# Performance work log

Measured on AMD Instinct MI355X. Metric: run time of the kernel, lower is better.

The kernel has to match this reference:

```python
import jax, jax.numpy as jnp
import numpy as np

EPS = 0.01       # l2-normalize epsilon
BN_EPS = 0.001   # batchnorm epsilon

def _l2norm(u):
    # tf.math.l2_normalize over axis=-2: x / sqrt(max(sum(x^2), eps))
    sq = jnp.sum(u * u, axis=-2, keepdims=True)
    return u / jnp.sqrt(jnp.maximum(sq, EPS))

def _dotprod(t, u):
    # einsum '...ij,...ik->...jk' contracting spatial axis, then flatten (C,C)->C*C
    d = jnp.einsum('bndi,bndj->bnij', t, _l2norm(u))
    return d.reshape(d.shape[0], d.shape[1], -1)

def _bn(x, gamma, beta):
    # inference-mode BN with moving_mean=0, moving_var=1 (fresh init)
    return gamma * (x / jnp.sqrt(1.0 + BN_EPS)) + beta

def setup_inputs() -> dict:
    key = jax.random.key(0)
    ks = jax.random.split(key, 9)
    B, N, D, C, BAS, U_IN, U_EQ = 8, 1024, 3, 64, 16, 512, 64
    F = 2 * C * C  # 8192 invariant features (2 input heads)
    t1 = jax.random.normal(ks[0], (B, N, D, C), dtype=jnp.float32)
    t2 = jax.random.normal(ks[1], (B, N, D, C), dtype=jnp.float32)
    u1 = jax.random.normal(ks[2], (B, N, D, C), dtype=jnp.float32)
    u2 = jax.random.normal(ks[3], (B, N, D, C), dtype=jnp.float32)
    V1 = jax.random.normal(ks[4], (B, N, D, BAS), dtype=jnp.float32)
    V2 = jax.random.normal(ks[5], (B, N, D, BAS), dtype=jnp.float32)
    W_inv = jax.random.normal(ks[6], (F, U_IN), dtype=jnp.float32) * 0.02
    b_inv = jnp.zeros((U_IN,), dtype=jnp.float32)
    g_inv = jnp.ones((U_IN,), dtype=jnp.float32)
    be_inv = jnp.zeros((U_IN,), dtype=jnp.float32)
    # two equivariant heads, each Dense(units=U_EQ*BAS)
    W_eq = jax.random.normal(ks[7], (2, F, U_EQ * BAS), dtype=jnp.float32) * 0.02
    b_eq = jnp.zeros((2, U_EQ * BAS), dtype=jnp.float32)
    g_eq = jnp.ones((2, U_EQ * BAS), dtype=jnp.float32)
    be_eq = jnp.zeros((2, U_EQ * BAS), dtype=jnp.float32)
    return {"t1": t1, "t2": t2, "u1": u1, "u2": u2, "V1": V1, "V2": V2,
            "W_inv": W_inv, "b_inv": b_inv, "g_inv": g_inv, "be_inv": be_inv,
            "W_eq": W_eq, "b_eq": b_eq, "g_eq": g_eq, "be_eq": be_eq}

def reference(t1, t2, u1, u2, V1, V2, W_inv, b_inv, g_inv, be_inv,
              W_eq, b_eq, g_eq, be_eq):
    # invariant features: concatenated flattened Gram blocks of the two heads
    feats = jnp.concatenate([_dotprod(t1, u1), _dotprod(t2, u2)], axis=-1)  # (B,N,F)
    # invariant branch: Dense -> BN -> ReLU
    invar = jax.nn.relu(_bn(feats @ W_inv + b_inv, g_inv, be_inv))  # (B,N,U_IN)
    # equivariant branch per head: Dense -> BN -> ReLU -> reshape -> basis recombine
    bas = V1.shape[-1]
    u_eq = W_eq.shape[-1] // bas
    eq_outs = []
    for l, V in enumerate((V1, V2)):
        wl = jax.nn.relu(_bn(feats @ W_eq[l] + b_eq[l], g_eq[l], be_eq[l]))
        wl = wl.reshape(wl.shape[0], wl.shape[1], u_eq, bas)  # (B,N,units,basis)
        # einsum '...ij,...mj->...mi': combine basis vectors -> (B,N,3,units)
        eq_outs.append(jnp.einsum('bnij,bnmj->bnmi', wl, V))
    eqvar = jnp.concatenate(eq_outs, axis=-1)  # (B,N,3,2*units)
    return invar, eqvar
```

## Files before the change

### kernel.cpp

```cpp
#include <hip/hip_runtime.h>
#include <hip/hip_bf16.h>

#define BROWS 8192
#define DDIM 3
#define CDIM 64
#define KF 8192
#define NINV 512
#define NEQ 1024
#define NTOT 2560
#define BAS 16
#define UEQ 64


typedef float f32x4 __attribute__((ext_vector_type(4)));
typedef __bf16 bf16x8_t __attribute__((ext_vector_type(8)));
typedef __bf16 bf16x4_t __attribute__((ext_vector_type(4)));

__device__ __forceinline__ void async_copy16(const void* g, void* l) {
    __builtin_amdgcn_global_load_lds(
        (__attribute__((address_space(1))) void*)(g),
        (__attribute__((address_space(3))) void*)(l), 16, 0, 0);
}

__global__ __launch_bounds__(256) void feats_kernel(
    const float* __restrict__ t1, const float* __restrict__ t2,
    const float* __restrict__ u1, const float* __restrict__ u2,
    __hip_bfloat16* __restrict__ feats)
{
    const int row = blockIdx.x;
    const int tid = threadIdx.x;
    __shared__ float sT[2 * DDIM * CDIM];
    __shared__ float sU[2 * DDIM * CDIM];

    const size_t base = (size_t)row * (DDIM * CDIM);
    if (tid < 192) {
        sT[tid]       = t1[base + tid];
        sT[192 + tid] = t2[base + tid];
        sU[tid]       = u1[base + tid];
        sU[192 + tid] = u2[base + tid];
    }
    __syncthreads();
    if (tid < 128) {
        const int h = tid >> 6, c = tid & 63;
        float* U = sU + h * 192;
        float sq = U[c] * U[c] + U[64 + c] * U[64 + c] + U[128 + c] * U[128 + c];
        float s = 1.0f / sqrtf(fmaxf(sq, 0.01f));
        U[c] *= s; U[64 + c] *= s; U[128 + c] *= s;
    }
    __syncthreads();
    const int h  = tid >> 7;
    const int i  = (tid >> 1) & 63;
    const int jh = (tid & 1) * 32;
    const float* T = sT + h * 192;
    const float* U = sU + h * 192;
    const float ti0 = T[i], ti1 = T[64 + i], ti2 = T[128 + i];

    const int kbase = h * 4096 + i * 64 + jh;
    const int kt    = kbase >> 5;
    const int mb    = row >> 8, rloc = row & 255;
    char* line = (char*)feats + (((size_t)(mb * 256 + kt)) << 14) + rloc * 64;

    #pragma unroll
    for (int g = 0; g < 4; ++g) {
        const int phys = (g + (rloc >> 1)) & 3;
        #pragma unroll
        for (int half = 0; half < 2; ++half) {
            const int j = jh + g * 8 + half * 4;
            const float4 u0 = *reinterpret_cast<const float4*>(U + j);
            const float4 u1 = *reinterpret_cast<const float4*>(U + 64 + j);
            const float4 u2 = *reinterpret_cast<const float4*>(U + 128 + j);
            bf16x4_t v;
            v[0] = (__bf16)(ti0 * u0.x + ti1 * u1.x + ti2 * u2.x);
            v[1] = (__bf16)(ti0 * u0.y + ti1 * u1.y + ti2 * u2.y);
            v[2] = (__bf16)(ti0 * u0.z + ti1 * u1.z + ti2 * u2.z);
            v[3] = (__bf16)(ti0 * u0.w + ti1 * u1.w + ti2 * u2.w);
            *reinterpret_cast<bf16x4_t*>(line + phys * 16 + half * 8) = v;
        }
    }
}

__global__ __launch_bounds__(256) void wt_kernel(
    const float* __restrict__ W_inv, const float* __restrict__ W_eq,
    __hip_bfloat16* __restrict__ WT)
{
    __shared__ float tile[32][33];
    const int tid = threadIdx.x;
    const int tx = tid & 31;
    const int ty = tid >> 5;
    const int n0 = blockIdx.x * 32;
    const int k0 = blockIdx.y * 32;

    const float* src; int ldn, nl0;
    if (n0 < NINV)            { src = W_inv;                       ldn = NINV; nl0 = n0; }
    else if (n0 < NINV + NEQ) { src = W_eq;                        ldn = NEQ;  nl0 = n0 - NINV; }
    else                      { src = W_eq + (size_t)KF * NEQ;     ldn = NEQ;  nl0 = n0 - NINV - NEQ; }

    #pragma unroll
    for (int i = 0; i < 4; ++i) {
        int kl = ty + i * 8;
        tile[kl][tx] = src[(size_t)(k0 + kl) * ldn + nl0 + tx];
    }
    __syncthreads();
    const int n_l = tid >> 3;
    const int k4  = (tid & 7) * 4;
    bf16x4_t v;
    #pragma unroll
    for (int q = 0; q < 4; ++q) v[q] = (__bf16)tile[k4 + q][n_l];

    const int n    = n0 + n_l;
    const int nb   = n >> 8, rloc = n & 255;
    const int kt   = k0 >> 5;
    const int lc   = (k4 >> 3) & 3, e = k4 & 7;
    const int phys = (lc + (rloc >> 1)) & 3;
    char* dst = (char*)WT + (((size_t)(nb * 256 + kt)) << 14)
              + rloc * 64 + phys * 16 + e * 2;
    *reinterpret_cast<bf16x4_t*>(dst) = v;
}

#define BM 256
#define BN 256
#define BK 32

struct GemmCtx {
    const char* pA;
    const char* pB;
    __hip_bfloat16* As[2];
    __hip_bfloat16* Bs[2];
    int soff;
    int chnk;
    int wm, wn, lane;
};

__device__ __forceinline__ void issue4(const GemmCtx& c, int buf, size_t toff) {
    #pragma unroll
    for (int j = 0; j < 2; ++j)
        async_copy16(c.pA + toff + c.soff + j * 8192,
                     (char*)c.As[buf] + c.soff + j * 8192);
    #pragma unroll
    for (int j = 0; j < 2; ++j)
        async_copy16(c.pB + toff + c.soff + j * 8192,
                     (char*)c.Bs[buf] + c.soff + j * 8192);
}

__device__ __forceinline__ void compute32(const GemmCtx& c, int buf, f32x4 (&acc)[4][8]) {
    const int l15 = c.lane & 15;
    bf16x8_t a[4], b[8];
    #pragma unroll
    for (int mt = 0; mt < 4; ++mt)
        a[mt] = *reinterpret_cast<const bf16x8_t*>(
            &c.As[buf][(c.wm + mt * 16 + l15) * BK + c.chnk]);
    #pragma unroll
    for (int nt = 0; nt < 8; ++nt)
        b[nt] = *reinterpret_cast<const bf16x8_t*>(
            &c.Bs[buf][(c.wn + nt * 16 + l15) * BK + c.chnk]);
    #pragma unroll
    for (int mt = 0; mt < 4; ++mt)
        #pragma unroll
        for (int nt = 0; nt < 8; ++nt)
            acc[mt][nt] = __builtin_amdgcn_mfma_f32_16x16x32_bf16(
                a[mt], b[nt], acc[mt][nt], 0, 0, 0);
}

__global__ __launch_bounds__(512, 2) void gemm_kernel(
    const __hip_bfloat16* __restrict__ A,
    const __hip_bfloat16* __restrict__ BT,
    const float* __restrict__ b_inv, const float* __restrict__ g_inv,
    const float* __restrict__ be_inv,
    const float* __restrict__ b_eq,  const float* __restrict__ g_eq,
    const float* __restrict__ be_eq,
    float* __restrict__ out_inv,
    float* __restrict__ Yeq)
{
    __shared__ alignas(16) __hip_bfloat16 AsBuf[2][BM * BK];
    __shared__ alignas(16) __hip_bfloat16 BsBuf[2][BN * BK];

    const int tid  = threadIdx.x;
    const int wave = tid >> 6;
    const int lane = tid & 63;

    const int b    = blockIdx.x;
    const int xcd  = b & 7;
    const int slot = b >> 3;
    const int nb   = slot % 10;
    const int mb   = xcd * 4 + slot / 10;
    const int n0   = nb * BN;
    const int m0   = mb * BM;

    GemmCtx c;
    c.wm   = (wave & 3) * 64;
    c.wn   = (wave >> 2) * 128;
    c.lane = lane;
    c.As[0] = &AsBuf[0][0]; c.As[1] = &AsBuf[1][0];
    c.Bs[0] = &BsBuf[0][0]; c.Bs[1] = &BsBuf[1][0];
    c.pA = (const char*)A  + ((size_t)mb << 22);
    c.pB = (const char*)BT + ((size_t)nb << 22);
    c.soff = tid * 16;
    c.chnk = (((lane >> 4) + ((lane & 15) >> 1)) & 3) * 8;

    f32x4 acc[4][8] = {};

    issue4(c, 0, 0);

    for (int kt = 0; kt < 256; kt += 2) {
        issue4(c, 1, ((size_t)(kt + 1)) << 14);
        asm volatile("s_waitcnt vmcnt(4)" ::: "memory");
        __builtin_amdgcn_s_barrier();
        asm volatile("" ::: "memory");
        compute32(c, 0, acc);
        asm volatile("" ::: "memory");
        __builtin_amdgcn_s_barrier();

        if (kt + 2 < 256) {
            issue4(c, 0, ((size_t)(kt + 2)) << 14);
            asm volatile("s_waitcnt vmcnt(4)" ::: "memory");
        } else {
            asm volatile("s_waitcnt vmcnt(0)" ::: "memory");
        }
        __builtin_amdgcn_s_barrier();
        asm volatile("" ::: "memory");
        compute32(c, 1, acc);
        asm volatile("" ::: "memory");
        __builtin_amdgcn_s_barrier();
    }

    const float RSQ = 0.9995003746877732f;
    #pragma unroll
    for (int nt = 0; nt < 8; ++nt) {
        const int gn = n0 + c.wn + nt * 16 + (lane & 15);
        float bbp, gg, bep;
        if (gn < NINV) {
            bbp = b_inv[gn]; gg = g_inv[gn]; bep = be_inv[gn];
        } else {
            const int e = gn - NINV, hh = e >> 10, nl = e & 1023;
            bbp = b_eq[hh * NEQ + nl]; gg = g_eq[hh * NEQ + nl]; bep = be_eq[hh * NEQ + nl];
        }
        gg *= RSQ;
        #pragma unroll
        for (int mt = 0; mt < 4; ++mt) {
            const int gmb = m0 + c.wm + mt * 16 + ((lane >> 4) << 2);
            #pragma unroll
            for (int rr = 0; rr < 4; ++rr) {
                float y = fmaxf(gg * (acc[mt][nt][rr] + bbp) + bep, 0.0f);
                const size_t gm = gmb + rr;
                if (gn < NINV) out_inv[gm * NINV + gn] = y;
                else           Yeq[gm * 2048 + (gn - NINV)] = y;
            }
        }
    }
}

__global__ __launch_bounds__(128) void eqcomb_kernel(
    const float* __restrict__ Yeq,
    const float* __restrict__ V1, const float* __restrict__ V2,
    float* __restrict__ out_eq)
{
    const int row = blockIdx.x;
    const int tid = threadIdx.x;
    __shared__ float sV[2][DDIM][BAS];
    if (tid < 96) {
        const int h = tid / 48, rem = tid % 48;
        const float* V = h ? V2 : V1;
        sV[h][rem / BAS][rem % BAS] = V[(size_t)row * (DDIM * BAS) + rem];
    }
    __syncthreads();
    const int l = tid >> 6, u = tid & 63;
    const float4* y4 = reinterpret_cast<const float4*>(
        Yeq + (size_t)row * 2048 + l * 1024 + u * BAS);
    float a0 = 0.f, a1 = 0.f, a2 = 0.f;
    #pragma unroll
    for (int q = 0; q < 4; ++q) {
        float4 w = y4[q];
        const float* v0 = sV[l][0] + q * 4;
        const float* v1 = sV[l][1] + q * 4;
        const float* v2 = sV[l][2] + q * 4;
        a0 += w.x * v0[0] + w.y * v0[1] + w.z * v0[2] + w.w * v0[3];
        a1 += w.x * v1[0] + w.y * v1[1] + w.z * v1[2] + w.w * v1[3];
        a2 += w.x * v2[0] + w.y * v2[1] + w.z * v2[2] + w.w * v2[3];
    }
    float* o = out_eq + (size_t)row * (DDIM * 128);
    o[0 * 128 + l * 64 + u] = a0;
    o[1 * 128 + l * 64 + u] = a1;
    o[2 * 128 + l * 64 + u] = a2;
}

extern "C" void kernel_launch(void* const* d_in, const int* in_sizes, int n_in,
                              void* d_out, int out_size, void* d_ws, size_t ws_size,
                              hipStream_t stream) {
    const float* t1    = (const float*)d_in[0];
    const float* t2    = (const float*)d_in[1];
    const float* u1    = (const float*)d_in[2];
    const float* u2    = (const float*)d_in[3];
    const float* V1    = (const float*)d_in[4];
    const float* V2    = (const float*)d_in[5];
    const float* W_inv = (const float*)d_in[6];
    const float* b_inv = (const float*)d_in[7];
    const float* g_inv = (const float*)d_in[8];
    const float* be_inv= (const float*)d_in[9];
    const float* W_eq  = (const float*)d_in[10];
    const float* b_eq  = (const float*)d_in[11];
    const float* g_eq  = (const float*)d_in[12];
    const float* be_eq = (const float*)d_in[13];
    float* out = (float*)d_out;

    char* ws = (char*)d_ws;
    __hip_bfloat16* feats = (__hip_bfloat16*)(ws);
    __hip_bfloat16* WT    = (__hip_bfloat16*)(ws + 134217728);
    float*          Yeq   = (float*)(ws + 176160768);

    float* out_inv = out;
    float* out_eq  = out + (size_t)BROWS * NINV;

    hipLaunchKernelGGL(feats_kernel, dim3(BROWS), dim3(256), 0, stream,
                       t1, t2, u1, u2, feats);
    hipLaunchKernelGGL(wt_kernel, dim3(NTOT / 32, KF / 32), dim3(256), 0, stream,
                       W_inv, W_eq, WT);
    hipLaunchKernelGGL(gemm_kernel, dim3((NTOT / BN) * (BROWS / BM)), dim3(512), 0, stream,
                       feats, WT, b_inv, g_inv, be_inv, b_eq, g_eq, be_eq,
                       out_inv, Yeq);
    hipLaunchKernelGGL(eqcomb_kernel, dim3(BROWS), dim3(128), 0, stream,
                       Yeq, V1, V2, out_eq);
}
```

Before: 625.1 us.

## Widen GEMM N-tile to 320 with 4-stage pipeline and split A/B loader waves

Changes the GEMM tile from 256x256 to 256x320, so the N=2560 dimension splits into 8 column blocks instead of 10 and each A tile is reused across more columns. The weight repack layout changes to match. The K-loop moves from double buffering to a 4-deep LDS ring with three tiles in flight, and waves 0-3 load A while waves 4-7 load B. Together this doubles LDS use and raises accumulator registers to 40 f32x4 per thread, which may hurt occupancy at 2 blocks per CU. The launch grid presumably shrinks to 256 blocks, which is not shown.

```diff
diff --git a/kernel.cpp b/kernel.cpp
--- a/kernel.cpp
+++ b/kernel.cpp
@@ -108,58 +108,20 @@
     for (int q = 0; q < 4; ++q) v[q] = (__bf16)tile[k4 + q][n_l];
 
     const int n    = n0 + n_l;
-    const int nb   = n >> 8, rloc = n & 255;
+    const int nb   = n / 320, rloc = n - nb * 320;
     const int kt   = k0 >> 5;
     const int lc   = (k4 >> 3) & 3, e = k4 & 7;
     const int phys = (lc + (rloc >> 1)) & 3;
-    char* dst = (char*)WT + (((size_t)(nb * 256 + kt)) << 14)
+    char* dst = (char*)WT + ((size_t)(nb * 256 + kt)) * 20480
               + rloc * 64 + phys * 16 + e * 2;
     *reinterpret_cast<bf16x4_t*>(dst) = v;
 }
 
 #define BM 256
-#define BN 256
+#define BN 320
 #define BK 32
-
-struct GemmCtx {
-    const char* pA;
-    const char* pB;
-    __hip_bfloat16* As[2];
-    __hip_bfloat16* Bs[2];
-    int soff;
-    int chnk;
-    int wm, wn, lane;
-};
-
-__device__ __forceinline__ void issue4(const GemmCtx& c, int buf, size_t toff) {
-    #pragma unroll
-    for (int j = 0; j < 2; ++j)
-        async_copy16(c.pA + toff + c.soff + j * 8192,
-                     (char*)c.As[buf] + c.soff + j * 8192);
-    #pragma unroll
-    for (int j = 0; j < 2; ++j)
-        async_copy16(c.pB + toff + c.soff + j * 8192,
-                     (char*)c.Bs[buf] + c.soff + j * 8192);
-}
-
-__device__ __forceinline__ void compute32(const GemmCtx& c, int buf, f32x4 (&acc)[4][8]) {
-    const int l15 = c.lane & 15;
-    bf16x8_t a[4], b[8];
-    #pragma unroll
-    for (int mt = 0; mt < 4; ++mt)
-        a[mt] = *reinterpret_cast<const bf16x8_t*>(
-            &c.As[buf][(c.wm + mt * 16 + l15) * BK + c.chnk]);
-    #pragma unroll
-    for (int nt = 0; nt < 8; ++nt)
-        b[nt] = *reinterpret_cast<const bf16x8_t*>(
-            &c.Bs[buf][(c.wn + nt * 16 + l15) * BK + c.chnk]);
-    #pragma unroll
-    for (int mt = 0; mt < 4; ++mt)
-        #pragma unroll
-        for (int nt = 0; nt < 8; ++nt)
-            acc[mt][nt] = __builtin_amdgcn_mfma_f32_16x16x32_bf16(
-                a[mt], b[nt], acc[mt][nt], 0, 0, 0);
-}
+#define ATILE 16384
+#define BTILE 20480
 
 __global__ __launch_bounds__(512, 2) void gemm_kernel(
     const __hip_bfloat16* __restrict__ A,
@@ -171,62 +133,127 @@
     float* __restrict__ out_inv,
     float* __restrict__ Yeq)
 {
-    __shared__ alignas(16) __hip_bfloat16 AsBuf[2][BM * BK];
-    __shared__ alignas(16) __hip_bfloat16 BsBuf[2][BN * BK];
+    __shared__ alignas(16) __hip_bfloat16 AsBuf[4][BM * BK];
+    __shared__ alignas(16) __hip_bfloat16 BsBuf[4][BN * BK];
 
     const int tid  = threadIdx.x;
     const int wave = tid >> 6;
     const int lane = tid & 63;
+    const bool aWave = wave < 4;
 
     const int b    = blockIdx.x;
     const int xcd  = b & 7;
     const int slot = b >> 3;
-    const int nb   = slot % 10;
-    const int mb   = xcd * 4 + slot / 10;
+    const int nb   = slot & 7;
+    const int mb   = xcd * 4 + (slot >> 3);
     const int n0   = nb * BN;
     const int m0   = mb * BM;
 
-    GemmCtx c;
-    c.wm   = (wave & 3) * 64;
-    c.wn   = (wave >> 2) * 128;
-    c.lane = lane;
-    c.As[0] = &AsBuf[0][0]; c.As[1] = &AsBuf[1][0];
-    c.Bs[0] = &BsBuf[0][0]; c.Bs[1] = &BsBuf[1][0];
-    c.pA = (const char*)A  + ((size_t)mb << 22);
-    c.pB = (const char*)BT + ((size_t)nb << 22);
-    c.soff = tid * 16;
-    c.chnk = (((lane >> 4) + ((lane & 15) >> 1)) & 3) * 8;
-
-    f32x4 acc[4][8] = {};
-
-    issue4(c, 0, 0);
-
-    for (int kt = 0; kt < 256; kt += 2) {
-        issue4(c, 1, ((size_t)(kt + 1)) << 14);
-        asm volatile("s_waitcnt vmcnt(4)" ::: "memory");
-        __builtin_amdgcn_s_barrier();
-        asm volatile("" ::: "memory");
-        compute32(c, 0, acc);
-        asm volatile("" ::: "memory");
-        __builtin_amdgcn_s_barrier();
-
-        if (kt + 2 < 256) {
-            issue4(c, 0, ((size_t)(kt + 2)) << 14);
-            asm volatile("s_waitcnt vmcnt(4)" ::: "memory");
-        } else {
-            asm volatile("s_waitcnt vmcnt(0)" ::: "memory");
-        }
-        __builtin_amdgcn_s_barrier();
-        asm volatile("" ::: "memory");
-        compute32(c, 1, acc);
-        asm volatile("" ::: "memory");
-        __builtin_amdgcn_s_barrier();
-    }
+    const char* pA = (const char*)A  + ((size_t)mb << 22);
+    const char* pB = (const char*)BT + (size_t)nb * 256 * BTILE;
+
+    const int aoff = wave * 4096 + lane * 16;
+    const int boff = (wave - 4) * 5120 + lane * 16;
+
+    const int chnk = (((lane >> 4) + ((lane & 15) >> 1)) & 3) * 8;
+    const int wm = (wave & 3) * 64;
+    const int wn = (wave >> 2) * 160;
+    const int l15 = lane & 15;
+
+    f32x4 acc[4][10] = {};
+
+#define ISSUE(bufi, t)                                                        \
+    do {                                                                      \
+        if (aWave) {                                                          \
+            _Pragma("unroll")                                                 \
+            for (int j = 0; j < 4; ++j)                                       \
+                async_copy16(pA + (size_t)(t) * ATILE + aoff + j * 1024,      \
+                             (char*)&AsBuf[bufi][0] + aoff + j * 1024);       \
+        } else {                                                              \
+            _Pragma("unroll")                                                 \
+            for (int j = 0; j < 5; ++j)                                       \
+                async_copy16(pB + (size_t)(t) * BTILE + boff + j * 1024,      \
+                             (char*)&BsBuf[bufi][0] + boff + j * 1024);       \
+        }                                                                     \
+    } while (0)
+
+#define COMPUTE(bufi)                                                         \
+    do {                                                                      \
+        bf16x8_t a_[4];                                                       \
+        _Pragma("unroll")                                                     \
+        for (int mt = 0; mt < 4; ++mt)                                        \
+            a_[mt] = *reinterpret_cast<const bf16x8_t*>(                      \
+                &AsBuf[bufi][(wm + mt * 16 + l15) * BK + chnk]);              \
+        _Pragma("unroll")                                                     \
+        for (int nt = 0; nt < 10; ++nt) {                                     \
+            bf16x8_t b_ = *reinterpret_cast<const bf16x8_t*>(                 \
+                &BsBuf[bufi][(wn + nt * 16 + l15) * BK + chnk]);              \
+            _Pragma("unroll")                                                 \
+            for (int mt = 0; mt < 4; ++mt)                                    \
+                acc[mt][nt] = __builtin_amdgcn_mfma_f32_16x16x32_bf16(        \
+                    a_[mt], b_, acc[mt][nt], 0, 0, 0);                        \
+        }                                                                     \
+    } while (0)
+
+#define WAITAB(na, nb_)                                                       \
+    do {                                                                      \
+        if (aWave) asm volatile("s_waitcnt vmcnt(" #na ")" ::: "memory");     \
+        else       asm volatile("s_waitcnt vmcnt(" #nb_ ")" ::: "memory");    \
+    } while (0)
+
+#define PHASE(bufc, bufp, t)                                                  \
+    do {                                                                      \
+        ISSUE(bufp, t + 3);                                                   \
+        WAITAB(12, 15);                                                       \
+        __builtin_amdgcn_s_barrier();                                         \
+        asm volatile("" ::: "memory");                                        \
+        COMPUTE(bufc);                                                        \
+        asm volatile("" ::: "memory");                                        \
+        __builtin_amdgcn_s_barrier();                                         \
+    } while (0)
+
+    ISSUE(0, 0);
+    ISSUE(1, 1);
+    ISSUE(2, 2);
+
+    for (int i4 = 0; i4 < 63; ++i4) {
+        const int t = i4 * 4;
+        PHASE(0, 3, t);
+        PHASE(1, 0, t + 1);
+        PHASE(2, 1, t + 2);
+        PHASE(3, 2, t + 3);
+    }
+    ISSUE(3, 255);
+    WAITAB(12, 15);
+    __builtin_amdgcn_s_barrier();
+    asm volatile("" ::: "memory");
+    COMPUTE(0);
+    asm volatile("" ::: "memory");
+    __builtin_amdgcn_s_barrier();
+
+    WAITAB(8, 10);
+    __builtin_amdgcn_s_barrier();
+    asm volatile("" ::: "memory");
+    COMPUTE(1);
+    asm volatile("" ::: "memory");
+    __builtin_amdgcn_s_barrier();
+
+    WAITAB(4, 5);
+    __builtin_amdgcn_s_barrier();
+    asm volatile("" ::: "memory");
+    COMPUTE(2);
+    asm volatile("" ::: "memory");
+    __builtin_amdgcn_s_barrier();
+
+    asm volatile("s_waitcnt vmcnt(0)" ::: "memory");
+    __builtin_amdgcn_s_barrier();
+    asm volatile("" ::: "memory");
+    COMPUTE(3);
 
     const float RSQ = 0.9995003746877732f;
     #pragma unroll
-    for (int nt = 0; nt < 8; ++nt) {
-        const int gn = n0 + c.wn + nt * 16 + (lane & 15);
+    for (int nt = 0; nt < 10; ++nt) {
+        const int gn = n0 + wn + nt * 16 + l15;
         float bbp, gg, bep;
         if (gn < NINV) {
             bbp = b_inv[gn]; gg = g_inv[gn]; bep = be_inv[gn];
@@ -237,7 +264,7 @@
         gg *= RSQ;
         #pragma unroll
         for (int mt = 0; mt < 4; ++mt) {
-            const int gmb = m0 + c.wm + mt * 16 + ((lane >> 4) << 2);
+            const int gmb = m0 + wm + mt * 16 + ((lane >> 4) << 2);
             #pragma unroll
             for (int rr = 0; rr < 4; ++rr) {
                 float y = fmaxf(gg * (acc[mt][nt][rr] + bbp) + bep, 0.0f);
@@ -247,6 +274,10 @@
             }
         }
     }
+#undef PHASE
+#undef WAITAB
+#undef COMPUTE
+#undef ISSUE
 }
 
 __global__ __launch_bounds__(128) void eqcomb_kernel(
```

Result: faster. 597.2 us (-4.5%).
